# Performance work log

Measured on AMD Instinct MI355X. Metric: run time of the kernel, lower is better.

The kernel has to match this reference:

```python
import jax, jax.numpy as jnp
import numpy as np

B, C, H, W = 8, 256, 48, 48
C8 = C // 8


def _conv1x1(w, b, t):
    # w: [O, C], b: [O], t: [B, C, H, W] -> [B, O, H, W]
    return jnp.einsum('oc,bchw->bohw', w, t) + b[None, :, None, None]


def setup_inputs() -> dict:
    key = jax.random.key(0)
    ks = jax.random.split(key, 16)
    s_qk = 1.0 / np.sqrt(C)
    inp = {
        'x': jax.random.normal(ks[0], (B, C, H, W), jnp.float32),
        'y': jax.random.normal(ks[1], (B, C, H, W), jnp.float32),
        'wqx': jax.random.normal(ks[2], (C8, C), jnp.float32) * s_qk,
        'bqx': jax.random.normal(ks[3], (C8,), jnp.float32) * 0.01,
        'wkx': jax.random.normal(ks[4], (C8, C), jnp.float32) * s_qk,
        'bkx': jax.random.normal(ks[5], (C8,), jnp.float32) * 0.01,
        'wvx': jax.random.normal(ks[6], (C, C), jnp.float32) * s_qk,
        'bvx': jax.random.normal(ks[7], (C,), jnp.float32) * 0.01,
        'wqy': jax.random.normal(ks[8], (C8, C), jnp.float32) * s_qk,
        'bqy': jax.random.normal(ks[9], (C8,), jnp.float32) * 0.01,
        'wky': jax.random.normal(ks[10], (C8, C), jnp.float32) * s_qk,
        'bky': jax.random.normal(ks[11], (C8,), jnp.float32) * 0.01,
        'wvy': jax.random.normal(ks[12], (C, C), jnp.float32) * s_qk,
        'bvy': jax.random.normal(ks[13], (C,), jnp.float32) * 0.01,
        'gamma_x': jax.random.normal(ks[14], (1,), jnp.float32) * 0.1,
        'gamma_y': jax.random.normal(ks[15], (1,), jnp.float32) * 0.1,
    }
    return inp


def reference(x, y, wqx, bqx, wkx, bkx, wvx, bvx, wqy, bqy, wky, bky, wvy, bvy, gamma_x, gamma_y):
    b, c, h, w = x.shape
    n = h * w
    # x-branch projections, flattened to [B, ch, N]
    q1 = _conv1x1(wqx, bqx, x).reshape(b, -1, n)  # [B, C8, N]
    k1 = _conv1x1(wkx, bkx, x).reshape(b, -1, n)
    v1 = _conv1x1(wvx, bvx, x).reshape(b, -1, n)  # [B, C, N]
    # y-branch
    q2 = _conv1x1(wqy, bqy, y).reshape(b, -1, n)
    k2 = _conv1x1(wky, bky, y).reshape(b, -1, n)
    v2 = _conv1x1(wvy, bvy, y).reshape(b, -1, n)
    # energy[b,i,j] = sum_c q[b,c,i]*k[b,c,j]; softmax over j (no 1/sqrt(d) scaling)
    attn1 = jax.nn.softmax(jnp.einsum('bci,bcj->bij', q1, k1), axis=-1)  # [B, N, N]
    attn2 = jax.nn.softmax(jnp.einsum('bci,bcj->bij', q2, k2), axis=-1)
    # cross value routing: out1 uses v1 with attn2^T, out2 uses v2 with attn1^T
    out1 = jnp.einsum('bcj,bij->bci', v1, attn2).reshape(b, c, h, w)
    out2 = jnp.einsum('bcj,bij->bci', v2, attn1).reshape(b, c, h, w)
    out1 = gamma_x * out1 + x
    out2 = gamma_y * out2 + y
    return (out1, out2)
```

## Files before the change

kernel.cpp:

```cpp
#include <hip/hip_runtime.h>
#include <math.h>

#define BB 8
#define CC 256
#define CQ 32
#define NN 2304
#define NT 36
#define NJ 36

typedef __attribute__((ext_vector_type(8))) short bf16x8;
typedef __attribute__((ext_vector_type(4))) float f32x4;
typedef __attribute__((ext_vector_type(4))) unsigned short u16x4;
typedef unsigned short ushort_t;
typedef unsigned int u32;

#define LOG2E 1.44269504088896f

static __device__ inline unsigned short f2bf(float f) {
    unsigned u = __builtin_bit_cast(unsigned, f);
    return (unsigned short)((u + 0x7fffu + ((u >> 16) & 1u)) >> 16);
}

static __device__ inline void gld_lds16(const ushort_t* g, ushort_t* l) {
    __builtin_amdgcn_global_load_lds(
        (const __attribute__((address_space(1))) u32*)g,
        (__attribute__((address_space(3))) u32*)l, 16, 0, 0);
}

#define S8  ((size_t)BB * NN * CQ)
#define SV  ((size_t)BB * NN * CC)
#define WOFF (4 * S8 + 2 * SV)

__global__ __launch_bounds__(256) void wcvt_kernel(
    const float* __restrict__ wqx, const float* __restrict__ bqx,
    const float* __restrict__ wkx, const float* __restrict__ bkx,
    const float* __restrict__ wvx, const float* __restrict__ bvx,
    const float* __restrict__ wqy, const float* __restrict__ bqy,
    const float* __restrict__ wky, const float* __restrict__ bky,
    const float* __restrict__ wvy, const float* __restrict__ bvy,
    ushort_t* __restrict__ ws)
{
    ushort_t* Wall = ws + WOFF;
    float*    ball = (float*)(ws + WOFF + 2 * 320 * 256);

    int id = blockIdx.x * 256 + threadIdx.x;
    int row = id >> 6;
    int c4  = (id & 63) * 4;
    int br  = row >= 320;
    int r   = row - br * 320;

    const float* src;
    float scale = 1.0f;
    if (r < 32)      { src = (br ? wqy : wqx) + (size_t)r * CC;        scale = LOG2E; }
    else if (r < 64) { src = (br ? wky : wkx) + (size_t)(r - 32) * CC; }
    else             { src = (br ? wvy : wvx) + (size_t)(r - 64) * CC; }

    float4 v = *(const float4*)(src + c4);
    u16x4 pk;
    pk[0] = f2bf(v.x * scale); pk[1] = f2bf(v.y * scale);
    pk[2] = f2bf(v.z * scale); pk[3] = f2bf(v.w * scale);
    int ch16 = c4 >> 3;
    int half = (c4 >> 2) & 1;
    int dcol = (((ch16 ^ (row & 7)) << 3) + (half << 2));
    *(u16x4*)(Wall + (size_t)row * CC + dcol) = pk;

    if (id < 640) {
        int row2 = id, br2 = row2 >= 320, r2 = row2 - br2 * 320;
        const float* bsrc; float sc2 = 1.0f;
        if (r2 < 32)      { bsrc = (br2 ? bqy : bqx) + r2;        sc2 = LOG2E; }
        else if (r2 < 64) { bsrc = (br2 ? bky : bkx) + (r2 - 32); }
        else              { bsrc = (br2 ? bvy : bvx) + (r2 - 64); }
        ball[row2] = bsrc[0] * sc2;
    }
}

__global__ __launch_bounds__(256, 3) void proj_kernel(
    const float* __restrict__ x, const float* __restrict__ y,
    ushort_t* __restrict__ ws)
{
    __shared__ __align__(16) ushort_t Wls[2][32 * 256];

    const int t = threadIdx.x, w = t >> 6, lane = t & 63;
    const int l15 = lane & 15, quad = lane >> 4;

    const int id   = blockIdx.x;
    const int b    = id & 7;
    const int rest = id >> 3;
    const int br   = rest >= NT;
    const int tile = br ? rest - NT : rest;

    const float* src = br ? y : x;
    const ushort_t* Wall = ws + WOFF + (size_t)br * 320 * CC;
    const float*    ball = (float*)(ws + WOFF + 2 * 320 * 256) + br * 320;

    ushort_t* qbuf = ws + (size_t)br * 2 * S8;
    ushort_t* kbuf = qbuf + S8;
    ushort_t* vbufg = ws + 4 * S8 + (size_t)br * SV;

    const int px0 = tile * 64 + w * 16;

#define STAGE_W(CH, BUF)                                                        \
    {                                                                           \
        const ushort_t* g = Wall + (size_t)(CH) * (32 * CC);                    \
        _Pragma("unroll")                                                       \
        for (int i = 0; i < 4; i++)                                             \
            gld_lds16(g + (size_t)(i * 256 + w * 64 + lane) * 8,                \
                      &Wls[BUF][(i * 256 + w * 64) * 8]);                       \
    }

    STAGE_W(0, 0)

    const float* ap = src + (size_t)b * CC * NN + px0 + l15;
    bf16x8 af[8];
#pragma unroll
    for (int q = 0; q < 8; q++) {
        float av[8];
#pragma unroll
        for (int j = 0; j < 8; j++)
            av[j] = ap[(size_t)(q * 32 + quad * 8 + j) * NN];
        union { bf16x8 v; unsigned short u[8]; } tmp;
#pragma unroll
        for (int j = 0; j < 8; j++) tmp.u[j] = f2bf(av[j]);
        af[q] = tmp.v;
    }

    f32x4 acc[20];
    const int rx = l15 & 7;

#define PROJ_CHUNK(CH, BUF)                                                     \
    {                                                                           \
        if ((CH) + 1 < 10) STAGE_W((CH) + 1, ((CH) + 1) & 1)                    \
        if ((CH) + 1 < 10) asm volatile("s_waitcnt vmcnt(4)" ::: "memory");     \
        else               asm volatile("s_waitcnt vmcnt(0)" ::: "memory");     \
        __builtin_amdgcn_s_barrier();                                           \
        const ushort_t* w0 = &Wls[BUF][(size_t)(0 * 16 + l15) * 256];           \
        const ushort_t* w1 = &Wls[BUF][(size_t)(1 * 16 + l15) * 256];           \
        f32x4 a0 = (f32x4){0.f, 0.f, 0.f, 0.f};                                 \
        f32x4 a1 = a0;                                                          \
        _Pragma("unroll")                                                       \
        for (int q = 0; q < 8; q++) {                                           \
            int co = ((q * 4 + quad) ^ rx) << 3;                                \
            bf16x8 b0 = *(const bf16x8*)(w0 + co);                              \
            bf16x8 b1 = *(const bf16x8*)(w1 + co);                              \
            a0 = __builtin_amdgcn_mfma_f32_16x16x32_bf16(af[q], b0, a0, 0,0,0); \
            a1 = __builtin_amdgcn_mfma_f32_16x16x32_bf16(af[q], b1, a1, 0,0,0); \
        }                                                                       \
        acc[(CH) * 2 + 0] = a0; acc[(CH) * 2 + 1] = a1;                         \
        __builtin_amdgcn_s_barrier();                                           \
    }

    PROJ_CHUNK(0, 0)
    PROJ_CHUNK(1, 1)
    PROJ_CHUNK(2, 0)
    PROJ_CHUNK(3, 1)
    PROJ_CHUNK(4, 0)
    PROJ_CHUNK(5, 1)
    PROJ_CHUNK(6, 0)
    PROJ_CHUNK(7, 1)
    PROJ_CHUNK(8, 0)
    PROJ_CHUNK(9, 1)
#undef PROJ_CHUNK
#undef STAGE_W

    ushort_t* scratch = &Wls[0][0];
#pragma unroll
    for (int ot = 0; ot < 4; ot++) {
        int o = ot * 16 + l15;
        float bias = ball[o];
        ushort_t* dst = (o < 32 ? qbuf : kbuf);
        int oc = o & 31;
#pragma unroll
        for (int r = 0; r < 4; r++) {
            int pxl = w * 16 + quad * 4 + r;
            dst[((size_t)b * NN + tile * 64 + pxl) * CQ + oc] = f2bf(acc[ot][r] + bias);
        }
    }
#pragma unroll
    for (int ot = 4; ot < 20; ot++) {
        int o_loc = (ot - 4) * 16 + l15;
        float bias = ball[64 + o_loc];
#pragma unroll
        for (int r = 0; r < 4; r++) {
            int pxl = w * 16 + quad * 4 + r;
            scratch[o_loc * 64 + (((pxl >> 3) ^ (o_loc & 7)) * 8) + (pxl & 7)] =
                f2bf(acc[ot][r] + bias);
        }
    }
    __syncthreads();
#pragma unroll
    for (int rep = 0; rep < 8; rep++) {
        int cid = rep * 256 + t;
        int o_loc = cid >> 3, pc = cid & 7;
        *(uint4*)(vbufg + ((size_t)b * CC + o_loc) * NN + tile * 64 + pc * 8) =
            *(uint4*)&scratch[cid * 8];
    }
}

#define TI 64
#define TJ 64

__global__ __launch_bounds__(256, 2) void flash_kernel(
    const float* __restrict__ x, const float* __restrict__ y,
    const float* __restrict__ gxp, const float* __restrict__ gyp,
    const ushort_t* __restrict__ ws, float* __restrict__ out)
{
    __shared__ __align__(16) ushort_t Vs[2][256 * 64];
    __shared__ __align__(16) ushort_t Ps[2][64 * 64];
    float* Lrow = (float*)&Ps[0][0];
    float* Ob   = (float*)&Vs[0][0];

    const int t = threadIdx.x, w = t >> 6, lane = t & 63;
    const int l15 = lane & 15, quad = lane >> 4;

    const int id   = blockIdx.x;
    const int b    = id & 7;
    const int rest = id >> 3;
    const int br   = rest >= NT;
    const int it   = br ? rest - NT : rest;
    const int i0   = it * TI;

    const ushort_t* Qb = ws + (br ? 0 : 2 * S8);
    const ushort_t* Kb = Qb + S8;
    const ushort_t* Vb = ws + 4 * S8 + (br ? SV : 0);
    const float* res = br ? y : x;
    const float gamma = br ? gyp[0] : gxp[0];
    float* op = out + (size_t)br * SV + (size_t)b * CC * NN;

    bf16x8 qf = *(const bf16x8*)(Qb + ((size_t)b * NN + i0 + w * 16 + l15) * CQ + quad * 8);

    f32x4 acc[4][4];
#pragma unroll
    for (int i = 0; i < 4; i++)
#pragma unroll
        for (int j = 0; j < 4; j++) acc[i][j] = (f32x4){0.f, 0.f, 0.f, 0.f};
    float l_loc[4] = {0.f, 0.f, 0.f, 0.f};

    const ushort_t* Vg = Vb + (size_t)b * CC * NN
                       + (size_t)(w * 64 + (lane >> 3)) * NN + (lane & 7) * 8;
    const ushort_t* kp = Kb + ((size_t)b * NN + l15) * CQ + quad * 8;

    {
        ushort_t* l = &Vs[0][(w * 64) * 64];
#pragma unroll
        for (int is = 0; is < 8; is++)
            gld_lds16(Vg + (size_t)is * 8 * NN, l + is * 512);
    }
    bf16x8 kfA[4], kfB[4];
#pragma unroll
    for (int n = 0; n < 4; n++)
        kfA[n] = *(const bf16x8*)(kp + (size_t)(n * 16) * CQ);
#pragma unroll
    for (int n = 0; n < 4; n++)
        kfB[n] = *(const bf16x8*)(kp + (size_t)(TJ + n * 16) * CQ);

    f32x4 sP[4];
#pragma unroll
    for (int n = 0; n < 4; n++)
        sP[n] = __builtin_amdgcn_mfma_f32_16x16x32_bf16(
                    qf, kfA[n], (f32x4){0.f, 0.f, 0.f, 0.f}, 0, 0, 0);

#define FLASH_ITER(JT, CUR, KFQK, KFLD)                                         \
    {                                                                           \
          \
        if ((JT) + 1 < NJ) {                                                    \
            ushort_t* l = &Vs[(CUR) ^ 1][(w * 64) * 64];                        \
            const ushort_t* g = Vg + (size_t)((JT) + 1) * TJ;                   \
            _Pragma("unroll")                                                   \
            for (int is = 0; is < 8; is++)                                      \
                gld_lds16(g + (size_t)is * 8 * NN, l + is * 512);               \
        }                                                                       \
                \
        if ((JT) + 2 < NJ) {                                                    \
            const ushort_t* kn = kp + (size_t)(((JT) + 2) * TJ) * CQ;           \
            _Pragma("unroll")                                                   \
            for (int n = 0; n < 4; n++)                                         \
                KFLD[n] = *(const bf16x8*)(kn + (size_t)(n * 16) * CQ);         \
        }                                                                       \
                   \
        unsigned short pu[4][4];                                                \
        _Pragma("unroll")                                                       \
        for (int n = 0; n < 4; n++)                                             \
            _Pragma("unroll")                                                   \
            for (int r = 0; r < 4; r++) {                                       \
                float p = __builtin_amdgcn_exp2f(sP[n][r]);                     \
                l_loc[r] += p;                                                  \
                pu[n][r] = f2bf(p);                                             \
            }                                                                   \
            \
        _Pragma("unroll")                                                       \
        for (int n = 0; n < 4; n++)                                             \
            _Pragma("unroll")                                                   \
            for (int r = 0; r < 4; r++) {                                       \
                int row = w * 16 + quad * 4 + r;                                \
                int ch  = (n * 2 + (l15 >> 3)) ^ (row & 7);                     \
                Ps[CUR][row * 64 + ch * 8 + (l15 & 7)] = pu[n][r];              \
            }                                                                   \
                    \
        if ((JT) + 1 < NJ) {                                                    \
            _Pragma("unroll")                                                   \
            for (int n = 0; n < 4; n++)                                         \
                sP[n] = __builtin_amdgcn_mfma_f32_16x16x32_bf16(                \
                    qf, KFQK[n], (f32x4){0.f, 0.f, 0.f, 0.f}, 0, 0, 0);         \
        }                                                                       \
                  \
        asm volatile("s_waitcnt lgkmcnt(0)" ::: "memory");                      \
        __builtin_amdgcn_s_barrier();                                           \
         \
        if ((JT) + 2 < NJ) asm volatile("s_waitcnt vmcnt(12)" ::: "memory");    \
        else               asm volatile("s_waitcnt vmcnt(0)"  ::: "memory");    \
                                            \
        _Pragma("unroll")                                                       \
        for (int ks = 0; ks < 2; ks++) {                                        \
            bf16x8 pf[4], vf[4];                                                \
            _Pragma("unroll")                                                   \
            for (int rt = 0; rt < 4; rt++) {                                    \
                int prow = rt * 16 + l15;                                       \
                int pch  = (ks * 4 + quad) ^ (l15 & 7);                         \
                pf[rt] = *(const bf16x8*)&Ps[CUR][prow * 64 + pch * 8];         \
            }                                                                   \
            _Pragma("unroll")                                                   \
            for (int ct = 0; ct < 4; ct++) {                                    \
                int row = w * 64 + ct * 16 + l15;                               \
                int pc  = (ks * 4 + quad) ^ (l15 & 7);                          \
                vf[ct] = *(const bf16x8*)&Vs[CUR][row * 64 + pc * 8];           \
            }                                                                   \
            __builtin_amdgcn_s_setprio(1);                                      \
            _Pragma("unroll")                                                   \
            for (int rt = 0; rt < 4; rt++)                                      \
                _Pragma("unroll")                                               \
                for (int ct = 0; ct < 4; ct++)                                  \
                    acc[rt][ct] = __builtin_amdgcn_mfma_f32_16x16x32_bf16(      \
                        pf[rt], vf[ct], acc[rt][ct], 0, 0, 0);                  \
            __builtin_amdgcn_s_setprio(0);                                      \
        }                                                                       \
    }

    for (int jt = 0; jt < NJ; jt += 2) {
        FLASH_ITER(jt,     0, kfB, kfA)
        FLASH_ITER(jt + 1, 1, kfA, kfB)
    }
#undef FLASH_ITER

#pragma unroll
    for (int r = 0; r < 4; r++) {
        float l = l_loc[r];
        l += __shfl_xor(l, 1);
        l += __shfl_xor(l, 2);
        l += __shfl_xor(l, 4);
        l += __shfl_xor(l, 8);
        l_loc[r] = l;
    }
    if (l15 == 0) {
        f32x4 lv = {l_loc[0], l_loc[1], l_loc[2], l_loc[3]};
        *(f32x4*)&Lrow[w * 16 + quad * 4] = lv;
    }
    __syncthreads();

    for (int rt = 0; rt < 4; rt++) {
        f32x4 lv = *(f32x4*)&Lrow[rt * 16 + quad * 4];
        f32x4 gi;
#pragma unroll
        for (int r = 0; r < 4; r++) gi[r] = gamma / lv[r];
#pragma unroll
        for (int ct = 0; ct < 4; ct++) {
            int c = w * 64 + ct * 16 + l15;
            f32x4 ov;
#pragma unroll
            for (int r = 0; r < 4; r++) ov[r] = acc[rt][ct][r] * gi[r];
            *(f32x4*)&Ob[c * 20 + quad * 4] = ov;
        }
        __syncthreads();
#pragma unroll
        for (int rep = 0; rep < 4; rep++) {
            int c  = rep * 64 + (t >> 2);
            int p4 = t & 3;
            f32x4 v = *(f32x4*)&Ob[c * 20 + p4 * 4];
            size_t go = ((size_t)b * CC + c) * NN + i0 + rt * 16 + p4 * 4;
            f32x4 r4 = *(const f32x4*)&res[go];
            v += r4;
            *(f32x4*)&op[(size_t)c * NN + i0 + rt * 16 + p4 * 4] = v;
        }
        __syncthreads();
    }
}

extern "C" void kernel_launch(void* const* d_in, const int* in_sizes, int n_in,
                              void* d_out, int out_size, void* d_ws, size_t ws_size,
                              hipStream_t stream)
{
    const float* x   = (const float*)d_in[0];
    const float* y   = (const float*)d_in[1];
    const float* wqx = (const float*)d_in[2];
    const float* bqx = (const float*)d_in[3];
    const float* wkx = (const float*)d_in[4];
    const float* bkx = (const float*)d_in[5];
    const float* wvx = (const float*)d_in[6];
    const float* bvx = (const float*)d_in[7];
    const float* wqy = (const float*)d_in[8];
    const float* bqy = (const float*)d_in[9];
    const float* wky = (const float*)d_in[10];
    const float* bky = (const float*)d_in[11];
    const float* wvy = (const float*)d_in[12];
    const float* bvy = (const float*)d_in[13];
    const float* gx  = (const float*)d_in[14];
    const float* gy  = (const float*)d_in[15];
    ushort_t* ws = (ushort_t*)d_ws;
    float* out = (float*)d_out;

    wcvt_kernel<<<dim3(160), 256, 0, stream>>>(wqx, bqx, wkx, bkx, wvx, bvx,
                                               wqy, bqy, wky, bky, wvy, bvy, ws);
    proj_kernel<<<dim3(576), 256, 0, stream>>>(x, y, ws);
    flash_kernel<<<dim3(576), 256, 0, stream>>>(x, y, gx, gy, ws, out);
}
```

Before: 210.8 us.

## Single-buffer V tile in LDS to raise occupancy to three blocks per CU

Drops the double-buffered V tile in shared memory, going from two 32KB buffers to one, and raises launch bounds from 2 to 3 blocks per CU. Each iteration now reads all V fragments into registers first, then issues the next tile's global-to-LDS load before the PV MFMAs so the load overlaps compute. K prefetch distance shrinks from two tiles to one. This trades intra-block pipelining depth, including a full vmcnt(0) wait every iteration and the extra vf registers, for more resident waves to hide latency.

```diff
diff --git a/kernel.cpp b/kernel.cpp
--- a/kernel.cpp
+++ b/kernel.cpp
@@ -199,15 +199,15 @@
 #define TI 64
 #define TJ 64
 
-__global__ __launch_bounds__(256, 2) void flash_kernel(
+__global__ __launch_bounds__(256, 3) void flash_kernel(
     const float* __restrict__ x, const float* __restrict__ y,
     const float* __restrict__ gxp, const float* __restrict__ gyp,
     const ushort_t* __restrict__ ws, float* __restrict__ out)
 {
-    __shared__ __align__(16) ushort_t Vs[2][256 * 64];
+    __shared__ __align__(16) ushort_t Vs[256 * 64];
     __shared__ __align__(16) ushort_t Ps[2][64 * 64];
     float* Lrow = (float*)&Ps[0][0];
-    float* Ob   = (float*)&Vs[0][0];
+    float* Ob   = (float*)&Vs[0];
 
     const int t = threadIdx.x, w = t >> 6, lane = t & 63;
     const int l15 = lane & 15, quad = lane >> 4;
@@ -240,41 +240,30 @@
     const ushort_t* kp = Kb + ((size_t)b * NN + l15) * CQ + quad * 8;
 
     {
-        ushort_t* l = &Vs[0][(w * 64) * 64];
+        ushort_t* l = &Vs[(w * 64) * 64];
 #pragma unroll
         for (int is = 0; is < 8; is++)
             gld_lds16(Vg + (size_t)is * 8 * NN, l + is * 512);
     }
-    bf16x8 kfA[4], kfB[4];
+    bf16x8 kf[4];
 #pragma unroll
     for (int n = 0; n < 4; n++)
-        kfA[n] = *(const bf16x8*)(kp + (size_t)(n * 16) * CQ);
-#pragma unroll
-    for (int n = 0; n < 4; n++)
-        kfB[n] = *(const bf16x8*)(kp + (size_t)(TJ + n * 16) * CQ);
+        kf[n] = *(const bf16x8*)(kp + (size_t)(n * 16) * CQ);
 
     f32x4 sP[4];
 #pragma unroll
     for (int n = 0; n < 4; n++)
         sP[n] = __builtin_amdgcn_mfma_f32_16x16x32_bf16(
-                    qf, kfA[n], (f32x4){0.f, 0.f, 0.f, 0.f}, 0, 0, 0);
-
-#define FLASH_ITER(JT, CUR, KFQK, KFLD)                                         \
+                    qf, kf[n], (f32x4){0.f, 0.f, 0.f, 0.f}, 0, 0, 0);
+
+#define FLASH_ITER(JT, CUR)                                                     \
     {                                                                           \
-          \
+                         \
         if ((JT) + 1 < NJ) {                                                    \
-            ushort_t* l = &Vs[(CUR) ^ 1][(w * 64) * 64];                        \
-            const ushort_t* g = Vg + (size_t)((JT) + 1) * TJ;                   \
-            _Pragma("unroll")                                                   \
-            for (int is = 0; is < 8; is++)                                      \
-                gld_lds16(g + (size_t)is * 8 * NN, l + is * 512);               \
-        }                                                                       \
-                \
-        if ((JT) + 2 < NJ) {                                                    \
-            const ushort_t* kn = kp + (size_t)(((JT) + 2) * TJ) * CQ;           \
+            const ushort_t* kn = kp + (size_t)(((JT) + 1) * TJ) * CQ;           \
             _Pragma("unroll")                                                   \
             for (int n = 0; n < 4; n++)                                         \
-                KFLD[n] = *(const bf16x8*)(kn + (size_t)(n * 16) * CQ);         \
+                kf[n] = *(const bf16x8*)(kn + (size_t)(n * 16) * CQ);           \
         }                                                                       \
                    \
         unsigned short pu[4][4];                                                \
@@ -295,49 +284,64 @@
                 int ch  = (n * 2 + (l15 >> 3)) ^ (row & 7);                     \
                 Ps[CUR][row * 64 + ch * 8 + (l15 & 7)] = pu[n][r];              \
             }                                                                   \
-                    \
+            \
         if ((JT) + 1 < NJ) {                                                    \
             _Pragma("unroll")                                                   \
             for (int n = 0; n < 4; n++)                                         \
                 sP[n] = __builtin_amdgcn_mfma_f32_16x16x32_bf16(                \
-                    qf, KFQK[n], (f32x4){0.f, 0.f, 0.f, 0.f}, 0, 0, 0);         \
+                    qf, kf[n], (f32x4){0.f, 0.f, 0.f, 0.f}, 0, 0, 0);           \
         }                                                                       \
-                  \
+                                   \
         asm volatile("s_waitcnt lgkmcnt(0)" ::: "memory");                      \
         __builtin_amdgcn_s_barrier();                                           \
-         \
-        if ((JT) + 2 < NJ) asm volatile("s_waitcnt vmcnt(12)" ::: "memory");    \
-        else               asm volatile("s_waitcnt vmcnt(0)"  ::: "memory");    \
-                                            \
+                \
+        asm volatile("s_waitcnt vmcnt(0)" ::: "memory");                        \
+                             \
+        bf16x8 vf[8];                                                           \
+        _Pragma("unroll")                                                       \
+        for (int ct = 0; ct < 4; ct++)                                          \
+            _Pragma("unroll")                                                   \
+            for (int ks = 0; ks < 2; ks++) {                                    \
+                int row = w * 64 + ct * 16 + l15;                               \
+                int pc  = (ks * 4 + quad) ^ (l15 & 7);                          \
+                vf[ks * 4 + ct] = *(const bf16x8*)&Vs[row * 64 + pc * 8];       \
+            }                                                                   \
+                         \
+        asm volatile("s_waitcnt lgkmcnt(0)" ::: "memory");                      \
+        __builtin_amdgcn_sched_barrier(0);                                      \
+                \
+        if ((JT) + 1 < NJ) {                                                    \
+            ushort_t* l = &Vs[(w * 64) * 64];                                   \
+            const ushort_t* g = Vg + (size_t)((JT) + 1) * TJ;                   \
+            _Pragma("unroll")                                                   \
+            for (int is = 0; is < 8; is++)                                      \
+                gld_lds16(g + (size_t)is * 8 * NN, l + is * 512);               \
+        }                                                                       \
+        __builtin_amdgcn_sched_barrier(0);                                      \
+                                       \
         _Pragma("unroll")                                                       \
         for (int ks = 0; ks < 2; ks++) {                                        \
-            bf16x8 pf[4], vf[4];                                                \
+            bf16x8 pf[4];                                                       \
             _Pragma("unroll")                                                   \
             for (int rt = 0; rt < 4; rt++) {                                    \
                 int prow = rt * 16 + l15;                                       \
                 int pch  = (ks * 4 + quad) ^ (l15 & 7);                         \
                 pf[rt] = *(const bf16x8*)&Ps[CUR][prow * 64 + pch * 8];         \
             }                                                                   \
-            _Pragma("unroll")                                                   \
-            for (int ct = 0; ct < 4; ct++) {                                    \
-                int row = w * 64 + ct * 16 + l15;                               \
-                int pc  = (ks * 4 + quad) ^ (l15 & 7);                          \
-                vf[ct] = *(const bf16x8*)&Vs[CUR][row * 64 + pc * 8];           \
-            }                                                                   \
             __builtin_amdgcn_s_setprio(1);                                      \
             _Pragma("unroll")                                                   \
             for (int rt = 0; rt < 4; rt++)                                      \
                 _Pragma("unroll")                                               \
                 for (int ct = 0; ct < 4; ct++)                                  \
                     acc[rt][ct] = __builtin_amdgcn_mfma_f32_16x16x32_bf16(      \
-                        pf[rt], vf[ct], acc[rt][ct], 0, 0, 0);                  \
+                        pf[rt], vf[ks * 4 + ct], acc[rt][ct], 0, 0, 0);         \
             __builtin_amdgcn_s_setprio(0);                                      \
         }                                                                       \
     }
 
     for (int jt = 0; jt < NJ; jt += 2) {
-        FLASH_ITER(jt,     0, kfB, kfA)
-        FLASH_ITER(jt + 1, 1, kfA, kfB)
+        FLASH_ITER(jt,     0)
+        FLASH_ITER(jt + 1, 1)
     }
 #undef FLASH_ITER
 
```

New measurement: 412.3 us. 1.96x slower.
